# Optimization experiments

Measured on AMD Instinct MI355X. Metric: run time of the kernel, lower is better.

Reference implementation:

```python
import jax, jax.numpy as jnp
import numpy as np

C = 256
H = 4
D = C // H
SCALE = D ** -0.5
EPS = 1e-5


def _lin(x, W, b):
    # torch nn.Linear: y = x @ W.T + b, W: [out, in]
    return x @ W.T + b


def _heads(x):
    B, N, _ = x.shape
    return x.reshape(B, N, H, D).transpose(0, 2, 1, 3)  # [B,H,N,D]


def _merge(x):
    B, h, N, d = x.shape
    return x.transpose(0, 2, 1, 3).reshape(B, N, h * d)


def _attn(q, k, v):
    # q,k,v: [B,H,N,D]; materializes [B,H,N,N] scores like the original
    scores = jnp.einsum('bhnd,bhmd->bhnm', q, k) * SCALE
    p = jax.nn.softmax(scores, axis=-1)
    return jnp.einsum('bhnm,bhmd->bhnd', p, v)


def setup_inputs() -> dict:
    key = jax.random.key(0)
    ks = jax.random.split(key, 20)
    B, N = 4, 4096
    s = 0.02
    inp = {
        'f_freq': jax.random.normal(ks[0], (B, N, C), jnp.float32),
        'f_spat': jax.random.normal(ks[1], (B, N, C), jnp.float32),
        'Wqf': jax.random.normal(ks[2], (C, C), jnp.float32) * s,
        'bqf': jnp.zeros((C,), jnp.float32),
        'Wks': jax.random.normal(ks[3], (C, C), jnp.float32) * s,
        'bks': jnp.zeros((C,), jnp.float32),
        'Wvs': jax.random.normal(ks[4], (C, C), jnp.float32) * s,
        'bvs': jnp.zeros((C,), jnp.float32),
        'Wqs': jax.random.normal(ks[5], (C, C), jnp.float32) * s,
        'bqs': jnp.zeros((C,), jnp.float32),
        'Wkf': jax.random.normal(ks[6], (C, C), jnp.float32) * s,
        'bkf': jnp.zeros((C,), jnp.float32),
        'Wvf': jax.random.normal(ks[7], (C, C), jnp.float32) * s,
        'bvf': jnp.zeros((C,), jnp.float32),
        'Wp': jax.random.normal(ks[8], (C, 2 * C), jnp.float32) * s,
        'bp': jnp.zeros((C,), jnp.float32),
        'gamma': jnp.ones((C,), jnp.float32),
        'beta': jnp.zeros((C,), jnp.float32),
    }
    return inp


def reference(f_freq, f_spat, Wqf, bqf, Wks, bks, Wvs, bvs, Wqs, bqs,
              Wkf, bkf, Wvf, bvf, Wp, bp, gamma, beta):
    # direction 1: freq queries attend to spatial keys/values
    q_f = _heads(_lin(f_freq, Wqf, bqf))
    k_s = _heads(_lin(f_spat, Wks, bks))
    v_s = _heads(_lin(f_spat, Wvs, bvs))
    out_f2s = _merge(_attn(q_f, k_s, v_s))
    # direction 2: spatial queries attend to freq keys/values
    q_s = _heads(_lin(f_spat, Wqs, bqs))
    k_f = _heads(_lin(f_freq, Wkf, bkf))
    v_f = _heads(_lin(f_freq, Wvf, bvf))
    out_s2f = _merge(_attn(q_s, k_f, v_f))
    fused = _lin(jnp.concatenate([out_f2s, out_s2f], axis=-1), Wp, bp)
    # LayerNorm over last dim
    mu = jnp.mean(fused, axis=-1, keepdims=True)
    var = jnp.var(fused, axis=-1, keepdims=True)
    fused = (fused - mu) * jax.lax.rsqrt(var + EPS) * gamma + beta
    return fused
```

## Files before the change

kernel.cpp:

```cpp
#include <hip/hip_runtime.h>
#include <hip/hip_bf16.h>

typedef __attribute__((ext_vector_type(4))) float floatx4;
typedef __attribute__((ext_vector_type(8))) short shortx8;

#define MFMA(a, b, c) __builtin_amdgcn_mfma_f32_16x16x32_bf16(a, b, c, 0, 0, 0)

static constexpr int MTOT = 16384;
static constexpr int NSEQ = 4096;
static constexpr int CD = 256;
static constexpr float SEXP = 0.18033688011112042f;

__device__ __forceinline__ unsigned short f2bf(float f) {
  unsigned int u = __float_as_uint(f);
  u += 0x7fffu + ((u >> 16) & 1u);
  return (unsigned short)(u >> 16);
}

__device__ __forceinline__ shortx8 ld8(const unsigned short* p) {
  return *reinterpret_cast<const shortx8*>(p);
}

__device__ __forceinline__ void gl_lds16(const unsigned short* g, unsigned short* l) {
  __builtin_amdgcn_global_load_lds(
      (const __attribute__((address_space(1))) unsigned int*)g,
      (__attribute__((address_space(3))) unsigned int*)l, 16, 0, 0);
}

struct CastArgs { const float* src[10]; };

__global__ __launch_bounds__(256) void cast_all(CastArgs a,
                                                unsigned short* __restrict__ xf,
                                                unsigned short* __restrict__ xs,
                                                unsigned short* __restrict__ wcat) {
  const int bx = blockIdx.x;
  const float* s;
  unsigned short* d;
  int off;
  if (bx < 8192) {
    const int which = bx >> 12;
    s = a.src[which];
    d = which ? xs : xf;
    off = (bx & 4095) * 1024 + threadIdx.x * 4;
  } else {
    const int w = bx - 8192;
    const int j = w >> 6;
    s = a.src[2 + j];
    d = wcat + j * 65536;
    off = (w & 63) * 1024 + threadIdx.x * 4;
  }
  float4 v = *reinterpret_cast<const float4*>(s + off);
  ushort4 o;
  o.x = f2bf(v.x); o.y = f2bf(v.y); o.z = f2bf(v.z); o.w = f2bf(v.w);
  *reinterpret_cast<ushort4*>(d + off) = o;
}

struct BiasPtrs { const float* p[6]; };

__global__ __launch_bounds__(256, 4) void qkv_gemm(const unsigned short* __restrict__ Xf,
                                                   const unsigned short* __restrict__ Xs,
                                                   const unsigned short* __restrict__ W6,
                                                   BiasPtrs bias6,
                                                   unsigned short* __restrict__ Yout) {
  __shared__ unsigned short smem[16384];
  const int j = blockIdx.y >> 1;
  const int o128 = (blockIdx.y & 1) * 128;
  const unsigned short* X = ((14 >> j) & 1) ? Xs : Xf;
  const unsigned short* W = W6 + j * 65536;
  const float* bias = bias6.p[j];
  const float sc = (j == 0 || j == 3) ? SEXP : 1.0f;
  unsigned short* Y = Yout + (size_t)j * MTOT * CD;

  const int wave = threadIdx.x >> 6, lane = threadIdx.x & 63;
  const int col = lane & 15, quad = lane >> 4;
  const int m0 = blockIdx.x * 128;
  const int mq = (wave & 1) * 64, oq = (wave >> 1) * 64;

  const int rA = lane >> 2, cA = lane & 3;
  const unsigned short* pA = X + (size_t)(m0 + wave * 32 + rA) * CD + cA * 8;
  const unsigned short* pB = W + (size_t)(o128 + wave * 32 + rA) * CD + cA * 8;
  unsigned short* lA = &smem[wave * 1024];
  unsigned short* lB = &smem[8192 + wave * 1024];

#define QSTAGE(BUF)                                   \
  do {                                                \
    gl_lds16(pA, lA + (BUF) * 4096);                  \
    gl_lds16(pA + 16 * CD, lA + (BUF) * 4096 + 512);  \
    gl_lds16(pB, lB + (BUF) * 4096);                  \
    gl_lds16(pB + 16 * CD, lB + (BUF) * 4096 + 512);  \
    pA += 32;                                         \
    pB += 32;                                         \
  } while (0)

  floatx4 acc[4][4];
  for (int mt = 0; mt < 4; ++mt)
    for (int f = 0; f < 4; ++f) acc[mt][f] = floatx4{0.f, 0.f, 0.f, 0.f};

  QSTAGE(0);
  __syncthreads();

  int buf = 0;
  for (int ks = 0; ks < 8; ++ks, buf ^= 1) {
    if (ks + 1 < 8) QSTAGE(buf ^ 1);
    shortx8 a[4], b[4];
    for (int mt = 0; mt < 4; ++mt)
      a[mt] = ld8(&smem[buf * 4096 + (mq + mt * 16 + col) * 32 + quad * 8]);
    for (int f = 0; f < 4; ++f)
      b[f] = ld8(&smem[8192 + buf * 4096 + (oq + f * 16 + col) * 32 + quad * 8]);
    for (int mt = 0; mt < 4; ++mt)
      for (int f = 0; f < 4; ++f)
        acc[mt][f] = MFMA(a[mt], b[f], acc[mt][f]);
    __syncthreads();
  }
#undef QSTAGE

  for (int mt = 0; mt < 4; ++mt)
    for (int f = 0; f < 4; ++f) {
      const int oc = o128 + oq + f * 16 + col;
      const float bv = bias[oc];
      for (int r = 0; r < 4; ++r)
        Y[(size_t)(m0 + mq + mt * 16 + quad * 4 + r) * CD + oc] =
            f2bf((acc[mt][f][r] + bv) * sc);
    }
}

__global__ __launch_bounds__(256) void vtrans(const unsigned short* __restrict__ qkv,
                                              unsigned short* __restrict__ Vt) {
  __shared__ unsigned short tile[64][65];
  const int pb = blockIdx.y;
  const int dir = pb >> 4, b = (pb >> 2) & 3, h = pb & 3;
  const size_t SZ = (size_t)MTOT * CD;
  const unsigned short* V = qkv + (size_t)dir * 3 * SZ + 2 * SZ;
  const int n0 = blockIdx.x * 64;
  const int t = threadIdx.x;
  const int dcol = t & 63, nrow = t >> 6;
  for (int nn = 0; nn < 64; nn += 4)
    tile[nn + nrow][dcol] = V[(size_t)(b * NSEQ + n0 + nn + nrow) * CD + h * 64 + dcol];
  __syncthreads();
  const int ncol = t & 63, drow = t >> 6;
  unsigned short* dst = Vt + (size_t)pb * 64 * NSEQ;
  for (int dd = 0; dd < 64; dd += 4)
    dst[(size_t)(dd + drow) * NSEQ + n0 + ncol] = tile[ncol][dd + drow];
}

__global__ __launch_bounds__(256, 4) void attn_kernel(const unsigned short* __restrict__ qkv,
                                                      const unsigned short* __restrict__ Vt,
                                                      unsigned short* __restrict__ Oout) {
  __shared__ unsigned short smem[16384];
  const size_t SZ = (size_t)MTOT * CD;
  const int pb = blockIdx.x & 31;
  const int xq = blockIdx.x >> 5;
  const int dir = pb >> 4, b = (pb >> 2) & 3, h4 = pb & 3;
  const unsigned short* Q = qkv + (size_t)dir * 3 * SZ;
  const unsigned short* K = Q + SZ;
  const unsigned short* VT = Vt + (size_t)pb * 64 * NSEQ;
  unsigned short* O = Oout + (size_t)dir * SZ;

  const int wave = threadIdx.x >> 6, lane = threadIdx.x & 63;
  const int col = lane & 15, quad = lane >> 4;
  const int rowbase = b * NSEQ;
  const int cb = h4 * 64;
  const int q0 = xq * 128 + wave * 32;

  shortx8 qf[2][2];
  for (int mt = 0; mt < 2; ++mt)
    for (int c = 0; c < 2; ++c)
      qf[mt][c] = ld8(Q + (size_t)(rowbase + q0 + mt * 16 + col) * CD + cb + c * 32 + quad * 8);

  floatx4 oacc[2][4];
  floatx4 lacc[2];
  for (int mt = 0; mt < 2; ++mt) {
    for (int d = 0; d < 4; ++d) oacc[mt][d] = floatx4{0.f, 0.f, 0.f, 0.f};
    lacc[mt] = floatx4{0.f, 0.f, 0.f, 0.f};
  }
  shortx8 ones;
  for (int i = 0; i < 8; ++i) ones[i] = (short)0x3F80;

  const int gp = 8 * (col >> 2) + (col & 3);
  const int swb = 2 * (col & 3);

  int kbase[2][2], vbase[2][4];
  for (int t = 0; t < 2; ++t)
    for (int c = 0; c < 2; ++c)
      kbase[t][c] = (gp + 4 * t) * 64 + ((c * 4 + quad + swb) & 7) * 8;
  for (int h = 0; h < 2; ++h)
    for (int db = 0; db < 4; ++db)
      vbase[h][db] = (db * 16 + col) * 64 + ((h * 4 + quad + swb) & 7) * 8;

  const int r8 = lane >> 3;
  const int cg = (lane - 2 * r8) & 7;

  const unsigned short* pk = K + (size_t)(rowbase + wave * 16 + r8) * CD + cb + cg * 8;
  const unsigned short* pv = VT + (size_t)(wave * 16 + r8) * NSEQ + cg * 8;
  unsigned short* lk = &smem[wave * 1024];
  unsigned short* lv = &smem[8192 + wave * 1024];

#define STAGE(BUF)                                  \
  do {                                              \
    gl_lds16(pk, lk + (BUF) * 4096);                \
    gl_lds16(pk + 8 * CD, lk + (BUF) * 4096 + 512); \
    gl_lds16(pv, lv + (BUF) * 4096);                \
    gl_lds16(pv + 8 * NSEQ, lv + (BUF) * 4096 + 512);\
    pk += 64 * CD;                                  \
    pv += 64;                                       \
  } while (0)

  STAGE(0);
  __syncthreads();

  int buf = 0;
  for (int kt = 0; kt < NSEQ; kt += 64, buf ^= 1) {
    if (kt + 64 < NSEQ) STAGE(buf ^ 1);

    for (int h = 0; h < 2; ++h) {
      shortx8 kf[2][2], vf[4];
      const int kb = buf * 4096 + h * 2048;
      for (int t = 0; t < 2; ++t)
        for (int c = 0; c < 2; ++c) kf[t][c] = ld8(&smem[kb + kbase[t][c]]);
      const int vb = 8192 + buf * 4096;
      for (int db = 0; db < 4; ++db) vf[db] = ld8(&smem[vb + vbase[h][db]]);

      for (int mt = 0; mt < 2; ++mt) {
        floatx4 z = floatx4{0.f, 0.f, 0.f, 0.f};
        floatx4 st0 = MFMA(kf[0][0], qf[mt][0], z);
        st0 = MFMA(kf[0][1], qf[mt][1], st0);
        floatx4 st1 = MFMA(kf[1][0], qf[mt][0], z);
        st1 = MFMA(kf[1][1], qf[mt][1], st1);
        float p[8];
        for (int r = 0; r < 4; ++r) {
          p[r]     = __builtin_amdgcn_exp2f(st0[r]);
          p[4 + r] = __builtin_amdgcn_exp2f(st1[r]);
        }
        union { shortx8 s8; unsigned int u[4]; } pu;
        for (int w = 0; w < 4; ++w)
          pu.u[w] = __builtin_amdgcn_perm(__float_as_uint(p[2 * w + 1]),
                                          __float_as_uint(p[2 * w]), 0x07060302u);
        lacc[mt] = MFMA(ones, pu.s8, lacc[mt]);
        for (int db = 0; db < 4; ++db)
          oacc[mt][db] = MFMA(vf[db], pu.s8, oacc[mt][db]);
      }
    }
    __syncthreads();
  }
#undef STAGE

  for (int mt = 0; mt < 2; ++mt) {
    const float inv = 1.0f / lacc[mt][0];
    for (int db = 0; db < 4; ++db) {
      ushort4 o4;
      o4.x = f2bf(oacc[mt][db][0] * inv);
      o4.y = f2bf(oacc[mt][db][1] * inv);
      o4.z = f2bf(oacc[mt][db][2] * inv);
      o4.w = f2bf(oacc[mt][db][3] * inv);
      *reinterpret_cast<ushort4*>(
          O + (size_t)(rowbase + q0 + mt * 16 + col) * CD + cb + db * 16 + quad * 4) = o4;
    }
  }
}

__global__ __launch_bounds__(256) void final_ln(const unsigned short* __restrict__ O1,
                                                const unsigned short* __restrict__ O2,
                                                const unsigned short* __restrict__ Wp,
                                                const float* __restrict__ bp,
                                                const float* __restrict__ gamma,
                                                const float* __restrict__ beta,
                                                float* __restrict__ out) {
  __shared__ float ssum[4][32], ssq[4][32];
  const int wave = threadIdx.x >> 6, lane = threadIdx.x & 63;
  const int col = lane & 15, quad = lane >> 4;
  const int m0 = blockIdx.x * 32;
  const int o0 = wave * 64;

  floatx4 acc[2][4];
  for (int mt = 0; mt < 2; ++mt)
    for (int f = 0; f < 4; ++f) acc[mt][f] = floatx4{0.f, 0.f, 0.f, 0.f};

  for (int kk = 0; kk < 16; ++kk) {
    const unsigned short* src = (kk < 8) ? O1 : O2;
    const int k0 = (kk & 7) * 32;
    shortx8 a[2], bb[4];
    for (int mt = 0; mt < 2; ++mt)
      a[mt] = ld8(src + (size_t)(m0 + mt * 16 + col) * CD + k0 + quad * 8);
    for (int f = 0; f < 4; ++f)
      bb[f] = ld8(Wp + (size_t)(o0 + f * 16 + col) * 512 + kk * 32 + quad * 8);
    for (int mt = 0; mt < 2; ++mt)
      for (int f = 0; f < 4; ++f)
        acc[mt][f] = MFMA(a[mt], bb[f], acc[mt][f]);
  }

  float vals[2][4][4];
  for (int mt = 0; mt < 2; ++mt)
    for (int f = 0; f < 4; ++f) {
      const float bv = bp[o0 + f * 16 + col];
      for (int r = 0; r < 4; ++r) vals[mt][f][r] = acc[mt][f][r] + bv;
    }

  for (int mt = 0; mt < 2; ++mt)
    for (int r = 0; r < 4; ++r) {
      float s = 0.f, q = 0.f;
      for (int f = 0; f < 4; ++f) { float v = vals[mt][f][r]; s += v; q += v * v; }
      for (int d = 1; d < 16; d <<= 1) { s += __shfl_xor(s, d); q += __shfl_xor(q, d); }
      if (col == 0) {
        ssum[wave][mt * 16 + quad * 4 + r] = s;
        ssq[wave][mt * 16 + quad * 4 + r] = q;
      }
    }
  __syncthreads();
  for (int mt = 0; mt < 2; ++mt)
    for (int r = 0; r < 4; ++r) {
      const int rl = mt * 16 + quad * 4 + r;
      const float S = ssum[0][rl] + ssum[1][rl] + ssum[2][rl] + ssum[3][rl];
      const float Qs = ssq[0][rl] + ssq[1][rl] + ssq[2][rl] + ssq[3][rl];
      const float mean = S * (1.0f / 256.0f);
      const float var = Qs * (1.0f / 256.0f) - mean * mean;
      const float rs = rsqrtf(var + 1e-5f);
      for (int f = 0; f < 4; ++f) {
        const int oc = o0 + f * 16 + col;
        out[(size_t)(m0 + rl) * CD + oc] = (vals[mt][f][r] - mean) * rs * gamma[oc] + beta[oc];
      }
    }
}

extern "C" void kernel_launch(void* const* d_in, const int* in_sizes, int n_in,
                              void* d_out, int out_size, void* d_ws, size_t ws_size,
                              hipStream_t stream) {
  const float* f_freq = (const float*)d_in[0];
  const float* f_spat = (const float*)d_in[1];
  const float* Wqf = (const float*)d_in[2];  const float* bqf = (const float*)d_in[3];
  const float* Wks = (const float*)d_in[4];  const float* bks = (const float*)d_in[5];
  const float* Wvs = (const float*)d_in[6];  const float* bvs = (const float*)d_in[7];
  const float* Wqs = (const float*)d_in[8];  const float* bqs = (const float*)d_in[9];
  const float* Wkf = (const float*)d_in[10]; const float* bkf = (const float*)d_in[11];
  const float* Wvf = (const float*)d_in[12]; const float* bvf = (const float*)d_in[13];
  const float* Wp  = (const float*)d_in[14]; const float* bp  = (const float*)d_in[15];
  const float* gamma = (const float*)d_in[16];
  const float* beta  = (const float*)d_in[17];
  float* out = (float*)d_out;

  const size_t SZ = (size_t)MTOT * CD;
  unsigned short* Xf  = (unsigned short*)d_ws;
  unsigned short* Xs  = Xf + SZ;
  unsigned short* W6  = Xs + SZ;
  unsigned short* WpB = W6 + 6 * 65536;
  unsigned short* QKV = WpB + 131072;
  unsigned short* O1  = QKV + 6 * SZ;
  unsigned short* O2  = O1 + SZ;
  unsigned short* Vt  = Xf;

  CastArgs ca = {{f_freq, f_spat, Wqf, Wks, Wvs, Wqs, Wkf, Wvf, Wp, Wp + 65536}};
  cast_all<<<8704, 256, 0, stream>>>(ca, Xf, Xs, W6);

  BiasPtrs bias6 = {{bqf, bks, bvs, bqs, bkf, bvf}};
  qkv_gemm<<<dim3(128, 12), 256, 0, stream>>>(Xf, Xs, W6, bias6, QKV);

  vtrans<<<dim3(64, 32), 256, 0, stream>>>(QKV, Vt);

  attn_kernel<<<1024, 256, 0, stream>>>(QKV, Vt, O1);

  final_ln<<<512, 256, 0, stream>>>(O1, O2, WpB, bp, gamma, beta, out);
}
```

Baseline: 303.3 us.

## Replace exp2 with Schraudolph bf16 bit-trick and fragment-major O/Wp layouts

The attention inner loop no longer calls exp2 and packs float halves. Each score is instead turned into integer bf16 bits with a multiply-add (x*128+16251), a Schraudolph-style approximation of 2^x that produces the bf16 P operand directly. Separately, the attention output and the projection weight Wp are stored in an MFMA-fragment-major layout, so final_ln loads contiguous 16-byte fragments per lane instead of strided rows. This cuts transcendental and pack work in the dominant kernel and makes the projection GEMM loads coalesced. The cost is a coarser exponential, with piecewise-linear error in the mantissa, and garbage bits if scores fall far below the representable range.

```diff
diff --git a/kernel.cpp b/kernel.cpp
--- a/kernel.cpp
+++ b/kernel.cpp
@@ -10,6 +10,8 @@
 static constexpr int NSEQ = 4096;
 static constexpr int CD = 256;
 static constexpr float SEXP = 0.18033688011112042f;
+static constexpr float SCH_A = 128.0f;
+static constexpr float SCH_B = 16251.0f;
 
 __device__ __forceinline__ unsigned short f2bf(float f) {
   unsigned int u = __float_as_uint(f);
@@ -27,32 +29,41 @@
       (__attribute__((address_space(3))) unsigned int*)l, 16, 0, 0);
 }
 
-struct CastArgs { const float* src[10]; };
+struct CastArgs { const float* src[9]; };
 
 __global__ __launch_bounds__(256) void cast_all(CastArgs a,
                                                 unsigned short* __restrict__ xf,
                                                 unsigned short* __restrict__ xs,
                                                 unsigned short* __restrict__ wcat) {
   const int bx = blockIdx.x;
-  const float* s;
-  unsigned short* d;
-  int off;
   if (bx < 8192) {
     const int which = bx >> 12;
-    s = a.src[which];
-    d = which ? xs : xf;
-    off = (bx & 4095) * 1024 + threadIdx.x * 4;
-  } else {
+    const float* s = a.src[which];
+    unsigned short* d = which ? xs : xf;
+    const int off = (bx & 4095) * 1024 + threadIdx.x * 4;
+    float4 v = *reinterpret_cast<const float4*>(s + off);
+    ushort4 o;
+    o.x = f2bf(v.x); o.y = f2bf(v.y); o.z = f2bf(v.z); o.w = f2bf(v.w);
+    *reinterpret_cast<ushort4*>(d + off) = o;
+  } else if (bx < 8576) {
     const int w = bx - 8192;
     const int j = w >> 6;
-    s = a.src[2 + j];
-    d = wcat + j * 65536;
-    off = (w & 63) * 1024 + threadIdx.x * 4;
-  }
-  float4 v = *reinterpret_cast<const float4*>(s + off);
-  ushort4 o;
-  o.x = f2bf(v.x); o.y = f2bf(v.y); o.z = f2bf(v.z); o.w = f2bf(v.w);
-  *reinterpret_cast<ushort4*>(d + off) = o;
+    const float* s = a.src[2 + j];
+    const int off = (w & 63) * 1024 + threadIdx.x * 4;
+    float4 v = *reinterpret_cast<const float4*>(s + off);
+    ushort4 o;
+    o.x = f2bf(v.x); o.y = f2bf(v.y); o.z = f2bf(v.z); o.w = f2bf(v.w);
+    *reinterpret_cast<ushort4*>(wcat + j * 65536 + off) = o;
+  } else {
+    const int flat = (bx - 8576) * 1024 + threadIdx.x * 4;
+    const int o = flat >> 9, k = flat & 511;
+    float4 v = *reinterpret_cast<const float4*>(a.src[8] + flat);
+    ushort4 q;
+    q.x = f2bf(v.x); q.y = f2bf(v.y); q.z = f2bf(v.z); q.w = f2bf(v.w);
+    const int idx = (((k >> 5) * 16 + (o >> 4)) * 64 + ((k >> 3) & 3) * 16 + (o & 15)) * 8
+                    + (k & 7);
+    *reinterpret_cast<ushort4*>(wcat + 6 * 65536 + idx) = q;
+  }
 }
 
 struct BiasPtrs { const float* p[6]; };
@@ -226,15 +237,14 @@
         st0 = MFMA(kf[0][1], qf[mt][1], st0);
         floatx4 st1 = MFMA(kf[1][0], qf[mt][0], z);
         st1 = MFMA(kf[1][1], qf[mt][1], st1);
-        float p[8];
+        int jj[8];
         for (int r = 0; r < 4; ++r) {
-          p[r]     = __builtin_amdgcn_exp2f(st0[r]);
-          p[4 + r] = __builtin_amdgcn_exp2f(st1[r]);
+          jj[r]     = (int)(st0[r] * SCH_A + SCH_B);
+          jj[4 + r] = (int)(st1[r] * SCH_A + SCH_B);
         }
         union { shortx8 s8; unsigned int u[4]; } pu;
         for (int w = 0; w < 4; ++w)
-          pu.u[w] = __builtin_amdgcn_perm(__float_as_uint(p[2 * w + 1]),
-                                          __float_as_uint(p[2 * w]), 0x07060302u);
+          pu.u[w] = (unsigned)jj[2 * w] | ((unsigned)jj[2 * w + 1] << 16);
         lacc[mt] = MFMA(ones, pu.s8, lacc[mt]);
         for (int db = 0; db < 4; ++db)
           oacc[mt][db] = MFMA(vf[db], pu.s8, oacc[mt][db]);
@@ -246,21 +256,25 @@
 
   for (int mt = 0; mt < 2; ++mt) {
     const float inv = 1.0f / lacc[mt][0];
+    const int mrow = rowbase + q0 + mt * 16;
     for (int db = 0; db < 4; ++db) {
+      const int dch = cb + db * 16 + quad * 4;
       ushort4 o4;
       o4.x = f2bf(oacc[mt][db][0] * inv);
       o4.y = f2bf(oacc[mt][db][1] * inv);
       o4.z = f2bf(oacc[mt][db][2] * inv);
       o4.w = f2bf(oacc[mt][db][3] * inv);
-      *reinterpret_cast<ushort4*>(
-          O + (size_t)(rowbase + q0 + mt * 16 + col) * CD + cb + db * 16 + quad * 4) = o4;
+      const size_t idx =
+          ((size_t)((mrow >> 4) * 8 + (dch >> 5)) * 64 + ((dch >> 3) & 3) * 16 + col) * 8
+          + (dch & 7);
+      *reinterpret_cast<ushort4*>(O + idx) = o4;
     }
   }
 }
 
 __global__ __launch_bounds__(256) void final_ln(const unsigned short* __restrict__ O1,
                                                 const unsigned short* __restrict__ O2,
-                                                const unsigned short* __restrict__ Wp,
+                                                const unsigned short* __restrict__ Wp2,
                                                 const float* __restrict__ bp,
                                                 const float* __restrict__ gamma,
                                                 const float* __restrict__ beta,
@@ -277,12 +291,11 @@
 
   for (int kk = 0; kk < 16; ++kk) {
     const unsigned short* src = (kk < 8) ? O1 : O2;
-    const int k0 = (kk & 7) * 32;
     shortx8 a[2], bb[4];
     for (int mt = 0; mt < 2; ++mt)
-      a[mt] = ld8(src + (size_t)(m0 + mt * 16 + col) * CD + k0 + quad * 8);
+      a[mt] = ld8(src + ((size_t)(((m0 + mt * 16) >> 4) * 8 + (kk & 7)) * 64 + lane) * 8);
     for (int f = 0; f < 4; ++f)
-      bb[f] = ld8(Wp + (size_t)(o0 + f * 16 + col) * 512 + kk * 32 + quad * 8);
+      bb[f] = ld8(Wp2 + ((size_t)(kk * 16 + wave * 4 + f) * 64 + lane) * 8);
     for (int mt = 0; mt < 2; ++mt)
       for (int f = 0; f < 4; ++f)
         acc[mt][f] = MFMA(a[mt], bb[f], acc[mt][f]);
@@ -347,7 +360,7 @@
   unsigned short* O2  = O1 + SZ;
   unsigned short* Vt  = Xf;
 
-  CastArgs ca = {{f_freq, f_spat, Wqf, Wks, Wvs, Wqs, Wkf, Wvf, Wp, Wp + 65536}};
+  CastArgs ca = {{f_freq, f_spat, Wqf, Wks, Wvs, Wqs, Wkf, Wvf, Wp}};
   cast_all<<<8704, 256, 0, stream>>>(ca, Xf, Xs, W6);
 
   BiasPtrs bias6 = {{bqf, bks, bvs, bqs, bkf, bvf}};
```

Result: no change. 297.9 us (-1.8%).
